# Optimization experiments

Hardware: AMD Instinct MI355X
Metric: run time of the kernel (lower is better)

Reference implementation:

```python
import jax, jax.numpy as jnp
import numpy as np

DIM = 192
HEADS = 8
B, H, W = 8, 128, 128

def _dwconv3x3(x, w):
    # x: [B,C,H,W], w: [C,1,3,3] depthwise
    return jax.lax.conv_general_dilated(
        x, w, window_strides=(1, 1), padding=((1, 1), (1, 1)),
        dimension_numbers=('NCHW', 'OIHW', 'NCHW'),
        feature_group_count=x.shape[1])

def _proj(x, pw, dw):
    # 1x1 pointwise (as einsum) followed by 3x3 depthwise
    y = jnp.einsum('bchw,oc->bohw', x, pw)
    return _dwconv3x3(y, dw)

def setup_inputs() -> dict:
    key = jax.random.key(0)
    ks = jax.random.split(key, 9)
    s_pw = 1.0 / np.sqrt(DIM)
    s_dw = 1.0 / 3.0
    return {
        'x_feat': jax.random.normal(ks[0], (B, DIM, H, W), jnp.float32),
        'y_feat': jax.random.normal(ks[1], (B, DIM, H, W), jnp.float32),
        'q_pw': jax.random.normal(ks[2], (DIM, DIM), jnp.float32) * s_pw,
        'q_dw': jax.random.normal(ks[3], (DIM, 1, 3, 3), jnp.float32) * s_dw,
        'k_pw': jax.random.normal(ks[4], (DIM, DIM), jnp.float32) * s_pw,
        'k_dw': jax.random.normal(ks[5], (DIM, 1, 3, 3), jnp.float32) * s_dw,
        'v_pw': jax.random.normal(ks[6], (DIM, DIM), jnp.float32) * s_pw,
        'v_dw': jax.random.normal(ks[7], (DIM, 1, 3, 3), jnp.float32) * s_dw,
        'proj_w': jax.random.normal(ks[8], (DIM, DIM), jnp.float32) * s_pw,
        'temperature': jnp.ones((HEADS, 1, 1), jnp.float32),
    }

def reference(x_feat, y_feat, q_pw, q_dw, k_pw, k_dw, v_pw, v_dw, proj_w, temperature):
    b, c, h, w = x_feat.shape
    ch = c // HEADS  # channels per head
    q = _proj(x_feat, q_pw, q_dw)
    k = _proj(y_feat, k_pw, k_dw)
    v = _proj(y_feat, v_pw, v_dw)
    # b (head c) h w -> b head c (h w)
    to_heads = lambda t: t.reshape(b, HEADS, ch, h * w)
    q, k, v = to_heads(q), to_heads(k), to_heads(v)
    # L2-normalize along token dim (torch F.normalize eps=1e-12)
    q = q / jnp.maximum(jnp.linalg.norm(q, axis=-1, keepdims=True), 1e-12)
    k = k / jnp.maximum(jnp.linalg.norm(k, axis=-1, keepdims=True), 1e-12)
    attn = jnp.einsum('bhcn,bhdn->bhcd', q, k) * temperature  # [b,heads,ch,ch]
    attn = jax.nn.softmax(attn, axis=-1)
    out = jnp.einsum('bhcd,bhdn->bhcn', attn, v)
    out = out.reshape(b, c, h, w)
    out = jnp.einsum('bchw,oc->bohw', out, proj_w)
    return out
```

## Files before the change

### kernel.cpp

```cpp
#include <hip/hip_runtime.h>
#include <hip/hip_bf16.h>

#define BATCH 8
#define CDIM 192
#define HEADS 8
#define CH 24
#define HH 128
#define WW 128
#define NPIX (HH*WW)
#define NELEM (BATCH*CDIM*NPIX)
#define NP4 (NPIX/4)

#define DSLAB 16
#define NJOBS 624

typedef __attribute__((ext_vector_type(8))) short bf16x8;
typedef __attribute__((ext_vector_type(4))) float f32x4;
typedef __attribute__((ext_vector_type(4))) unsigned int u32x4;
typedef __attribute__((ext_vector_type(4))) unsigned short u16x4;
typedef unsigned int u32;
typedef const __attribute__((address_space(1))) u32* gas_ptr;
typedef __attribute__((address_space(3))) u32* las_ptr;

#define UNIT 100663296ull
__device__ __align__(256) unsigned char g_pool[4 * UNIT + (16u << 20)];

#define OFF_T0   (0 * UNIT)
#define OFF_QB   (1 * UNIT)
#define OFF_KB   (2 * UNIT)
#define OFF_V    (3 * UNIT)
#define OFF_MISC (4 * UNIT)
#define OFF_PART (OFF_MISC)
#define OFF_S    (OFF_MISC + 2555904ull)
#define OFF_M    (OFF_S + 159744ull)
#define OFF_MF   (OFF_M + 1179648ull)

__device__ inline unsigned short bf_rne(float x) {
  unsigned u = __float_as_uint(x);
  unsigned r = (u + 0x7fffu + ((u >> 16) & 1u)) >> 16;
  return (unsigned short)r;
}
__device__ inline void f32_split(float x, unsigned short& h, unsigned short& l) {
  h = bf_rne(x);
  float hf = __uint_as_float(((unsigned)h) << 16);
  l = bf_rne(x - hf);
}

__global__ __launch_bounds__(64) void w_to_frag(const float* __restrict__ W,
                                                unsigned short* __restrict__ F,
                                                int nb) {
  const int b = blockIdx.x / 12, mf = blockIdx.x % 12;
  const int lane = threadIdx.x;
  const int row = mf * 16 + (lane & 15);
  const size_t lo = (size_t)nb * CDIM * CDIM;
#pragma unroll
  for (int ks = 0; ks < 6; ++ks) {
    const int k0 = ks * 32 + (lane >> 4) * 8;
    const float* src = W + ((size_t)b * CDIM + row) * CDIM + k0;
    bf16x8 hv, lv;
#pragma unroll
    for (int j = 0; j < 8; ++j) {
      unsigned short h, l;
      f32_split(src[j], h, l);
      hv[j] = (short)h;
      lv[j] = (short)l;
    }
    const size_t didx = (((size_t)(blockIdx.x) * 6 + ks) * 64 + lane) * 8;
    *(bf16x8*)(F + didx) = hv;
    *(bf16x8*)(F + lo + didx) = lv;
  }
}

__global__ __launch_bounds__(256, 2) void mfma_gemm192(
    const float* __restrict__ X,
    const unsigned short* __restrict__ WF, size_t w_lo,
    int w_bstride,
    float* __restrict__ Out) {
  const int bn = blockIdx.x;
  const int b = blockIdx.y;
  const int t = threadIdx.x;
  const int lane = t & 63, wid = t >> 6;
  const int wm = wid >> 1, wn = wid & 1;
  const int kq = lane >> 4;

  __shared__ float Xs[2][32][128];

  const size_t wbase = (size_t)b * w_bstride;
  const float* Xb = X + (size_t)b * CDIM * NPIX + bn * 128;
  const int pxl = wn * 64 + (lane & 15);

  int srow[4], scol4[4];
#pragma unroll
  for (int p = 0; p < 4; ++p) {
    const int f = (wid * 4 + p) * 64 + lane;
    srow[p] = f >> 5;
    scol4[p] = (f & 31) ^ (((srow[p] >> 3) & 1) << 2);
  }

  f32x4 acc[6][4];
#pragma unroll
  for (int mi = 0; mi < 6; ++mi)
#pragma unroll
    for (int ni = 0; ni < 4; ++ni) acc[mi][ni] = (f32x4){0.f, 0.f, 0.f, 0.f};

#pragma unroll
  for (int p = 0; p < 4; ++p) {
    const float* src = Xb + (size_t)(srow[p]) * NPIX + scol4[p] * 4;
    las_ptr dst = (las_ptr)(void*)(&Xs[0][0][0] + (wid * 4 + p) * 256);
    __builtin_amdgcn_global_load_lds((gas_ptr)(const void*)src, dst, 16, 0, 0);
  }
  __syncthreads();

  int cur = 0;
  for (int ks = 0; ks < 6; ++ks) {
    if (ks < 5) {
#pragma unroll
      for (int p = 0; p < 4; ++p) {
        const float* src =
            Xb + (size_t)((ks + 1) * 32 + srow[p]) * NPIX + scol4[p] * 4;
        las_ptr dst =
            (las_ptr)(void*)(&Xs[cur ^ 1][0][0] + (wid * 4 + p) * 256);
        __builtin_amdgcn_global_load_lds((gas_ptr)(const void*)src, dst, 16, 0, 0);
      }
    }

    bf16x8 Ah[6], Al[6];
#pragma unroll
    for (int mi = 0; mi < 6; ++mi) {
      const int mf = wm * 6 + mi;
      const size_t idx = wbase + (((size_t)(mf * 6 + ks)) * 64 + lane) * 8;
      Ah[mi] = *(const bf16x8*)(WF + idx);
      Al[mi] = *(const bf16x8*)(WF + w_lo + idx);
    }

    u32x4 Bh[4], Bl[4];
#pragma unroll
    for (int ni = 0; ni < 4; ++ni) {
      const int pxs = (pxl + ni * 16) ^ ((kq & 1) << 4);
#pragma unroll
      for (int jp = 0; jp < 4; ++jp) {
        const float x0 = Xs[cur][kq * 8 + 2 * jp][pxs];
        const float x1 = Xs[cur][kq * 8 + 2 * jp + 1][pxs];
        const unsigned u0 = __float_as_uint(x0);
        const unsigned u1 = __float_as_uint(x1);
        Bh[ni][jp] = (u1 & 0xffff0000u) | (u0 >> 16);
        const float rr0 = x0 - __uint_as_float(u0 & 0xffff0000u);
        const float rr1 = x1 - __uint_as_float(u1 & 0xffff0000u);
        Bl[ni][jp] = ((unsigned)bf_rne(rr1) << 16) | (unsigned)bf_rne(rr0);
      }
    }

#pragma unroll
    for (int mi = 0; mi < 6; ++mi)
#pragma unroll
      for (int ni = 0; ni < 4; ++ni) {
        const bf16x8 bh = __builtin_bit_cast(bf16x8, Bh[ni]);
        const bf16x8 bl = __builtin_bit_cast(bf16x8, Bl[ni]);
        acc[mi][ni] = __builtin_amdgcn_mfma_f32_16x16x32_bf16(
            Ah[mi], bh, acc[mi][ni], 0, 0, 0);
        acc[mi][ni] = __builtin_amdgcn_mfma_f32_16x16x32_bf16(
            Ah[mi], bl, acc[mi][ni], 0, 0, 0);
        acc[mi][ni] = __builtin_amdgcn_mfma_f32_16x16x32_bf16(
            Al[mi], bh, acc[mi][ni], 0, 0, 0);
      }

    __syncthreads();
    cur ^= 1;
  }

  const int ocol = bn * 128 + wn * 64 + (lane & 15);
  const int orow = wm * 96 + (lane >> 4) * 4;
#pragma unroll
  for (int mi = 0; mi < 6; ++mi)
#pragma unroll
    for (int r = 0; r < 4; ++r) {
      const int och = orow + mi * 16 + r;
      float* dst = Out + ((size_t)b * CDIM + och) * NPIX + ocol;
#pragma unroll
      for (int ni = 0; ni < 4; ++ni) dst[ni * 16] = acc[mi][ni][r];
    }
}

__global__ __launch_bounds__(256) void dwconv(const float* __restrict__ In,
                                              const float* __restrict__ Wd,
                                              float* __restrict__ Out) {
  const int idx = blockIdx.x * 256 + threadIdx.x;
  if (idx >= NELEM / 4) return;
  const int x4 = (idx & 31) * 4;
  const int y = (idx >> 5) & 127;
  const int c = (idx >> 12) % CDIM;
  const int b = idx / (32 * 128 * CDIM);

  const float* base = In + (size_t)(b * CDIM + c) * NPIX;
  float w[9];
#pragma unroll
  for (int i = 0; i < 9; ++i) w[i] = Wd[c * 9 + i];

  float acc0 = 0.f, acc1 = 0.f, acc2 = 0.f, acc3 = 0.f;
#pragma unroll
  for (int dy = 0; dy < 3; ++dy) {
    const int yy = y + dy - 1;
    if (yy < 0 || yy > 127) continue;
    const float* row = base + yy * WW;
    float vb0 = (x4 > 0) ? row[x4 - 1] : 0.f;
    const float4 m = *(const float4*)(row + x4);
    const float vb5 = (x4 + 4 < WW) ? row[x4 + 4] : 0.f;
    const float w0 = w[dy * 3 + 0], w1 = w[dy * 3 + 1], w2 = w[dy * 3 + 2];
    acc0 += w0 * vb0 + w1 * m.x + w2 * m.y;
    acc1 += w0 * m.x + w1 * m.y + w2 * m.z;
    acc2 += w0 * m.y + w1 * m.z + w2 * m.w;
    acc3 += w0 * m.z + w1 * m.w + w2 * vb5;
  }
  float4 o;
  o.x = acc0; o.y = acc1; o.z = acc2; o.w = acc3;
  *(float4*)(Out + (size_t)idx * 4) = o;
}

__global__ __launch_bounds__(256) void dwconv_bf(const float* __restrict__ In,
                                                 const float* __restrict__ Wd,
                                                 unsigned short* __restrict__ Out) {
  const int idx = blockIdx.x * 256 + threadIdx.x;
  if (idx >= NELEM / 4) return;
  const int x4 = (idx & 31) * 4;
  const int y = (idx >> 5) & 127;
  const int c = (idx >> 12) % CDIM;
  const int b = idx / (32 * 128 * CDIM);

  const float* base = In + (size_t)(b * CDIM + c) * NPIX;
  float w[9];
#pragma unroll
  for (int i = 0; i < 9; ++i) w[i] = Wd[c * 9 + i];

  float a[4] = {0.f, 0.f, 0.f, 0.f};
#pragma unroll
  for (int dy = 0; dy < 3; ++dy) {
    const int yy = y + dy - 1;
    if (yy < 0 || yy > 127) continue;
    const float* row = base + yy * WW;
    float vb0 = (x4 > 0) ? row[x4 - 1] : 0.f;
    const float4 m = *(const float4*)(row + x4);
    const float vb5 = (x4 + 4 < WW) ? row[x4 + 4] : 0.f;
    const float w0 = w[dy * 3 + 0], w1 = w[dy * 3 + 1], w2 = w[dy * 3 + 2];
    a[0] += w0 * vb0 + w1 * m.x + w2 * m.y;
    a[1] += w0 * m.x + w1 * m.y + w2 * m.z;
    a[2] += w0 * m.y + w1 * m.z + w2 * m.w;
    a[3] += w0 * m.z + w1 * m.w + w2 * vb5;
  }
  u16x4 hv, lv;
#pragma unroll
  for (int j = 0; j < 4; ++j) {
    unsigned short h, l;
    f32_split(a[j], h, l);
    hv[j] = h;
    lv[j] = l;
  }
  *(u16x4*)(Out + (size_t)idx * 4) = hv;
  *(u16x4*)(Out + NELEM + (size_t)idx * 4) = lv;
}

__global__ __launch_bounds__(256) void dots_mfma(
    const unsigned short* __restrict__ QF,
    const unsigned short* __restrict__ KF,
    float* __restrict__ Part) {
  const int bh = blockIdx.x;
  const int slab = blockIdx.y;
  const int b = bh >> 3, h = bh & 7;
  const int t = threadIdx.x;
  const int lane = t & 63, wid = t >> 6;

  const size_t rowbase = (size_t)(b * CDIM + h * CH);
  const int px0 = slab * 1024 + wid * 256;
  const int rr = lane & 15;
  const int j8 = (lane >> 4) * 8;

  f32x4 accx[2][2], aqq[2], aqhl[2], akk[2], akhl[2];
#pragma unroll
  for (int mi = 0; mi < 2; ++mi) {
#pragma unroll
    for (int ni = 0; ni < 2; ++ni) accx[mi][ni] = (f32x4){0.f, 0.f, 0.f, 0.f};
    aqq[mi] = (f32x4){0.f, 0.f, 0.f, 0.f};
    aqhl[mi] = (f32x4){0.f, 0.f, 0.f, 0.f};
    akk[mi] = (f32x4){0.f, 0.f, 0.f, 0.f};
    akhl[mi] = (f32x4){0.f, 0.f, 0.f, 0.f};
  }

#pragma unroll
  for (int s = 0; s < 8; ++s) {
    const int px = px0 + s * 32 + j8;
    bf16x8 qh[2], ql[2], kh[2], kl[2];
#pragma unroll
    for (int mi = 0; mi < 2; ++mi) {
      const size_t off = (rowbase + mi * 16 + rr) * (size_t)NPIX + px;
      qh[mi] = *(const bf16x8*)(QF + off);
      ql[mi] = *(const bf16x8*)(QF + NELEM + off);
      kh[mi] = *(const bf16x8*)(KF + off);
      kl[mi] = *(const bf16x8*)(KF + NELEM + off);
    }
#pragma unroll
    for (int mi = 0; mi < 2; ++mi) {
#pragma unroll
      for (int ni = 0; ni < 2; ++ni) {
        accx[mi][ni] = __builtin_amdgcn_mfma_f32_16x16x32_bf16(
            qh[mi], kh[ni], accx[mi][ni], 0, 0, 0);
        accx[mi][ni] = __builtin_amdgcn_mfma_f32_16x16x32_bf16(
            qh[mi], kl[ni], accx[mi][ni], 0, 0, 0);
        accx[mi][ni] = __builtin_amdgcn_mfma_f32_16x16x32_bf16(
            ql[mi], kh[ni], accx[mi][ni], 0, 0, 0);
      }
      aqq[mi] = __builtin_amdgcn_mfma_f32_16x16x32_bf16(qh[mi], qh[mi],
                                                        aqq[mi], 0, 0, 0);
      aqhl[mi] = __builtin_amdgcn_mfma_f32_16x16x32_bf16(qh[mi], ql[mi],
                                                         aqhl[mi], 0, 0, 0);
      akk[mi] = __builtin_amdgcn_mfma_f32_16x16x32_bf16(kh[mi], kh[mi],
                                                        akk[mi], 0, 0, 0);
      akhl[mi] = __builtin_amdgcn_mfma_f32_16x16x32_bf16(kh[mi], kl[mi],
                                                         akhl[mi], 0, 0, 0);
    }
  }

  __shared__ float xls[4][24][24];
  __shared__ float qls[4][24], kls[4][24];
  const int col = lane & 15;
  const int rbase = (lane >> 4) * 4;
#pragma unroll
  for (int mi = 0; mi < 2; ++mi) {
#pragma unroll
    for (int ni = 0; ni < 2; ++ni) {
      const int d = ni * 16 + col;
      if (d < 24) {
#pragma unroll
        for (int r = 0; r < 4; ++r) {
          const int c = mi * 16 + rbase + r;
          if (c < 24) xls[wid][c][d] = accx[mi][ni][r];
        }
      }
    }
    const int cc = mi * 16 + col;
    const int rd = col - rbase;
    if (cc < 24 && rd >= 0 && rd < 4) {
      qls[wid][cc] = aqq[mi][rd] + 2.f * aqhl[mi][rd];
      kls[wid][cc] = akk[mi][rd] + 2.f * akhl[mi][rd];
    }
  }
  __syncthreads();

  float* P = Part + ((size_t)bh * DSLAB + slab) * NJOBS;
  for (int j = t; j < 576; j += 256) {
    const int c = j / 24, d = j % 24;
    P[j] = xls[0][c][d] + xls[1][c][d] + xls[2][c][d] + xls[3][c][d];
  }
  if (t < 24) P[576 + t] = qls[0][t] + qls[1][t] + qls[2][t] + qls[3][t];
  else if (t >= 32 && t < 56) {
    const int c = t - 32;
    P[600 + c] = kls[0][c] + kls[1][c] + kls[2][c] + kls[3][c];
  }
}

__global__ __launch_bounds__(640) void dots_reduce(const float* __restrict__ Part,
                                                   float* __restrict__ S) {
  const int bh = blockIdx.x;
  const int job = threadIdx.x;
  if (job >= NJOBS) return;
  float s = 0.f;
  for (int i = 0; i < DSLAB; ++i)
    s += Part[((size_t)bh * DSLAB + i) * NJOBS + job];
  S[bh * NJOBS + job] = s;
}

__global__ __launch_bounds__(576) void build_M(const float* __restrict__ S,
                                               const float* __restrict__ PW,
                                               const float* __restrict__ Temp,
                                               float* __restrict__ M) {
  const int b = blockIdx.x, h = blockIdx.y;
  const int bh = b * 8 + h;
  __shared__ float att[CH][CH];
  __shared__ float qn[CH], kn[CH];
  const int t = threadIdx.x;
  const float* Sb = S + (size_t)bh * NJOBS;

  if (t < CH) {
    qn[t] = fmaxf(sqrtf(Sb[576 + t]), 1e-12f);
    kn[t] = fmaxf(sqrtf(Sb[600 + t]), 1e-12f);
  }
  __syncthreads();
  const float temp = Temp[h];
  if (t < 576) {
    const int c = t / 24, d = t % 24;
    att[c][d] = Sb[t] / (qn[c] * kn[d]) * temp;
  }
  __syncthreads();
  if (t < CH) {
    float mx = -1e30f;
    for (int d = 0; d < CH; ++d) mx = fmaxf(mx, att[t][d]);
    float sum = 0.f;
    for (int d = 0; d < CH; ++d) {
      const float e = __expf(att[t][d] - mx);
      att[t][d] = e;
      sum += e;
    }
    const float inv = 1.f / sum;
    for (int d = 0; d < CH; ++d) att[t][d] *= inv;
  }
  __syncthreads();
  for (int i = t; i < CDIM * CH; i += 576) {
    const int o = i / CH, d = i % CH;
    float s = 0.f;
#pragma unroll
    for (int c = 0; c < CH; ++c) s += PW[o * CDIM + h * CH + c] * att[c][d];
    M[((size_t)b * CDIM + o) * CDIM + h * CH + d] = s;
  }
}


extern "C" void kernel_launch(void* const* d_in, const int* in_sizes, int n_in,
                              void* d_out, int out_size, void* d_ws, size_t ws_size,
                              hipStream_t stream) {
  const float* x_feat = (const float*)d_in[0];
  const float* y_feat = (const float*)d_in[1];
  const float* q_pw   = (const float*)d_in[2];
  const float* q_dw   = (const float*)d_in[3];
  const float* k_pw   = (const float*)d_in[4];
  const float* k_dw   = (const float*)d_in[5];
  const float* v_pw   = (const float*)d_in[6];
  const float* v_dw   = (const float*)d_in[7];
  const float* proj_w = (const float*)d_in[8];
  const float* temp   = (const float*)d_in[9];
  float* out = (float*)d_out;

  unsigned char* pool;
  (void)hipGetSymbolAddress((void**)&pool, HIP_SYMBOL(g_pool));
  float* t0 = (float*)(pool + OFF_T0);
  unsigned short* QB = (unsigned short*)(pool + OFF_QB);
  unsigned short* KB = (unsigned short*)(pool + OFF_KB);
  float* v  = (float*)(pool + OFF_V);
  float* part = (float*)(pool + OFF_PART);
  float* S    = (float*)(pool + OFF_S);
  float* M    = (float*)(pool + OFF_M);
  unsigned short* MF = (unsigned short*)(pool + OFF_MF);

  unsigned short* WQF = MF + 2ull * 8 * CDIM * CDIM;
  unsigned short* WKF = WQF + 2ull * CDIM * CDIM;
  unsigned short* WVF = WKF + 2ull * CDIM * CDIM;

  const size_t w1_lo = (size_t)1 * CDIM * CDIM;
  const size_t w8_lo = (size_t)8 * CDIM * CDIM;

  const dim3 ggrid(NPIX / 128, BATCH);
  const int dwgrid = (NELEM / 4) / 256;

  w_to_frag<<<12, 64, 0, stream>>>(q_pw, WQF, 1);
  w_to_frag<<<12, 64, 0, stream>>>(k_pw, WKF, 1);
  w_to_frag<<<12, 64, 0, stream>>>(v_pw, WVF, 1);

  mfma_gemm192<<<ggrid, 256, 0, stream>>>(x_feat, WQF, w1_lo, 0, t0);
  dwconv_bf<<<dwgrid, 256, 0, stream>>>(t0, q_dw, QB);
  mfma_gemm192<<<ggrid, 256, 0, stream>>>(y_feat, WKF, w1_lo, 0, t0);
  dwconv_bf<<<dwgrid, 256, 0, stream>>>(t0, k_dw, KB);

  dots_mfma<<<dim3(64, DSLAB), 256, 0, stream>>>(QB, KB, part);
  dots_reduce<<<64, 640, 0, stream>>>(part, S);
  build_M<<<dim3(BATCH, HEADS), 576, 0, stream>>>(S, proj_w, temp, M);
  w_to_frag<<<8 * 12, 64, 0, stream>>>(M, MF, 8);

  mfma_gemm192<<<ggrid, 256, 0, stream>>>(y_feat, WVF, w1_lo, 0, t0);
  dwconv<<<dwgrid, 256, 0, stream>>>(t0, v_dw, v);

  mfma_gemm192<<<ggrid, 256, 0, stream>>>(v, MF, w8_lo, CDIM * CDIM, out);
}
```

Baseline: 455.1 us.

## Replace double-buffered direct-to-LDS loads with single-buffer register-staged loads

The pointwise GEMM's X tile loading moves from double-buffered global_load_lds prefetch to plain float4 global loads into registers, followed by stores into a single padded LDS buffer. A second barrier after the B-fragment reads lets the MFMA phase run while other waves start the next loads. This halves LDS use, which may allow more resident blocks, but it gives up explicit prefetch overlap and adds a barrier per K step. It likely reverts to a simpler earlier scheme.

```diff
diff --git a/kernel.cpp b/kernel.cpp
--- a/kernel.cpp
+++ b/kernel.cpp
@@ -18,9 +18,6 @@
 typedef __attribute__((ext_vector_type(4))) float f32x4;
 typedef __attribute__((ext_vector_type(4))) unsigned int u32x4;
 typedef __attribute__((ext_vector_type(4))) unsigned short u16x4;
-typedef unsigned int u32;
-typedef const __attribute__((address_space(1))) u32* gas_ptr;
-typedef __attribute__((address_space(3))) u32* las_ptr;
 
 #define UNIT 100663296ull
 __device__ __align__(256) unsigned char g_pool[4 * UNIT + (16u << 20)];
@@ -83,46 +80,30 @@
   const int wm = wid >> 1, wn = wid & 1;
   const int kq = lane >> 4;
 
-  __shared__ float Xs[2][32][128];
+  __shared__ float Xs[32][132];
 
   const size_t wbase = (size_t)b * w_bstride;
-  const float* Xb = X + (size_t)b * CDIM * NPIX + bn * 128;
+  const float* Xb = X + (size_t)b * CDIM * NPIX;
+  const int col4 = (t & 31) * 4;
+  const int r0 = t >> 5;
   const int pxl = wn * 64 + (lane & 15);
 
-  int srow[4], scol4[4];
-#pragma unroll
-  for (int p = 0; p < 4; ++p) {
-    const int f = (wid * 4 + p) * 64 + lane;
-    srow[p] = f >> 5;
-    scol4[p] = (f & 31) ^ (((srow[p] >> 3) & 1) << 2);
-  }
-
   f32x4 acc[6][4];
 #pragma unroll
   for (int mi = 0; mi < 6; ++mi)
 #pragma unroll
     for (int ni = 0; ni < 4; ++ni) acc[mi][ni] = (f32x4){0.f, 0.f, 0.f, 0.f};
 
-#pragma unroll
-  for (int p = 0; p < 4; ++p) {
-    const float* src = Xb + (size_t)(srow[p]) * NPIX + scol4[p] * 4;
-    las_ptr dst = (las_ptr)(void*)(&Xs[0][0][0] + (wid * 4 + p) * 256);
-    __builtin_amdgcn_global_load_lds((gas_ptr)(const void*)src, dst, 16, 0, 0);
-  }
-  __syncthreads();
-
-  int cur = 0;
   for (int ks = 0; ks < 6; ++ks) {
-    if (ks < 5) {
-#pragma unroll
-      for (int p = 0; p < 4; ++p) {
-        const float* src =
-            Xb + (size_t)((ks + 1) * 32 + srow[p]) * NPIX + scol4[p] * 4;
-        las_ptr dst =
-            (las_ptr)(void*)(&Xs[cur ^ 1][0][0] + (wid * 4 + p) * 256);
-        __builtin_amdgcn_global_load_lds((gas_ptr)(const void*)src, dst, 16, 0, 0);
-      }
-    }
+    float4 st[4];
+#pragma unroll
+    for (int p = 0; p < 4; ++p)
+      st[p] = *(const float4*)(Xb + (size_t)(ks * 32 + r0 + 8 * p) * NPIX +
+                               bn * 128 + col4);
+#pragma unroll
+    for (int p = 0; p < 4; ++p)
+      *(float4*)&Xs[r0 + 8 * p][col4 ^ ((p & 1) << 4)] = st[p];
+    __syncthreads();
 
     bf16x8 Ah[6], Al[6];
 #pragma unroll
@@ -139,8 +120,8 @@
       const int pxs = (pxl + ni * 16) ^ ((kq & 1) << 4);
 #pragma unroll
       for (int jp = 0; jp < 4; ++jp) {
-        const float x0 = Xs[cur][kq * 8 + 2 * jp][pxs];
-        const float x1 = Xs[cur][kq * 8 + 2 * jp + 1][pxs];
+        const float x0 = Xs[kq * 8 + 2 * jp][pxs];
+        const float x1 = Xs[kq * 8 + 2 * jp + 1][pxs];
         const unsigned u0 = __float_as_uint(x0);
         const unsigned u1 = __float_as_uint(x1);
         Bh[ni][jp] = (u1 & 0xffff0000u) | (u0 >> 16);
@@ -149,6 +130,7 @@
         Bl[ni][jp] = ((unsigned)bf_rne(rr1) << 16) | (unsigned)bf_rne(rr0);
       }
     }
+    __syncthreads();
 
 #pragma unroll
     for (int mi = 0; mi < 6; ++mi)
@@ -163,9 +145,6 @@
         acc[mi][ni] = __builtin_amdgcn_mfma_f32_16x16x32_bf16(
             Al[mi], bh, acc[mi][ni], 0, 0, 0);
       }
-
-    __syncthreads();
-    cur ^= 1;
   }
 
   const int ocol = bn * 128 + wn * 64 + (lane & 15);
```

Result: no change. 446.5 us (-1.9%).
